# Kernel tuning notes

Hardware: AMD Instinct MI355X
Metric: run time of the kernel (lower is better)

Reference implementation:

```python
import jax, jax.numpy as jnp
import numpy as np

N = 100_000      # nodes
E = 1_600_000    # directed edges (avg degree 16)
F_IN = 128       # num_node_features
H = 8            # heads in conv1
C = 32           # hidden_channels
G = 64           # graphs in batch
NC = 10          # num_classes


def setup_inputs() -> dict:
    key = jax.random.key(0)
    ks = jax.random.split(key, 12)
    gl = lambda k, shape, fan: (jax.random.normal(k, shape, jnp.float32) / np.sqrt(fan)).astype(jnp.float32)
    return {
        "x": jax.random.normal(ks[0], (N, F_IN), jnp.float32),
        "edge_index": jax.random.randint(ks[1], (2, E), 0, N, dtype=jnp.int32),
        "batch": jnp.sort(jax.random.randint(ks[2], (N,), 0, G, dtype=jnp.int32)),
        "W1": gl(ks[3], (F_IN, H * C), F_IN),
        "att_src1": gl(ks[4], (H, C), C),
        "att_dst1": gl(ks[5], (H, C), C),
        "b1": jnp.zeros((H * C,), jnp.float32),
        "W2": gl(ks[6], (H * C, C), H * C),
        "att_src2": gl(ks[7], (1, C), C),
        "att_dst2": gl(ks[8], (1, C), C),
        "b2": jnp.zeros((C,), jnp.float32),
        "Wlin": gl(ks[9], (C, NC), C),
        "blin": jnp.zeros((NC,), jnp.float32),
    }


def gat_conv(x, src, dst, W, att_src, att_dst, bias, heads, ch, concat):
    """PyG GATConv (eval mode): gather, LeakyReLU(0.2) scores, segment softmax over dst, scatter-sum."""
    n = x.shape[0]
    h = (x @ W).reshape(n, heads, ch)                     # [N,H,C]
    a_s = jnp.sum(h * att_src, axis=-1)                   # [N,H]
    a_d = jnp.sum(h * att_dst, axis=-1)                   # [N,H]
    e = jax.nn.leaky_relu(a_s[src] + a_d[dst], 0.2)       # [E,H]
    m = jax.ops.segment_max(e, dst, num_segments=n)       # [N,H], stable softmax
    p = jnp.exp(e - m[dst])
    z = jax.ops.segment_sum(p, dst, num_segments=n)
    coef = p / (z[dst] + 1e-16)                           # [E,H]
    out = jax.ops.segment_sum(coef[:, :, None] * h[src], dst, num_segments=n)  # [N,H,C]
    out = out.reshape(n, heads * ch) if concat else out.mean(axis=1)
    return out + bias


def reference(x, edge_index, batch, W1, att_src1, att_dst1, b1,
              W2, att_src2, att_dst2, b2, Wlin, blin):
    n = x.shape[0]
    loops = jnp.arange(n, dtype=edge_index.dtype)         # GATConv add_self_loops=True
    src = jnp.concatenate([edge_index[0], loops])
    dst = jnp.concatenate([edge_index[1], loops])

    h = gat_conv(x, src, dst, W1, att_src1, att_dst1, b1, H, C, concat=True)
    h = jax.nn.elu(h)                                     # dropout is identity in eval
    h = gat_conv(h, src, dst, W2, att_src2, att_dst2, b2, 1, C, concat=False)

    # global_mean_pool over graph ids
    sums = jax.ops.segment_sum(h, batch, num_segments=G)  # [G,C]
    cnts = jax.ops.segment_sum(jnp.ones((n,), h.dtype), batch, num_segments=G)
    pooled = sums / jnp.maximum(cnts, 1.0)[:, None]

    return pooled @ Wlin + blin                           # [G,NC]
```

## Files before the change

### kernel.cpp

```cpp
#include <hip/hip_runtime.h>
#include <cstdint>

#define NN 100000
#define EE 1600000
#define GG 64
#define FIN 128
#define HC 256
#define NC 10

typedef short v8s __attribute__((ext_vector_type(8)));
typedef float v4f __attribute__((ext_vector_type(4)));

static __device__ __forceinline__ float lrelu(float x) { return x > 0.f ? x : 0.2f * x; }
static __device__ __forceinline__ float bf2f(unsigned short b) {
  return __uint_as_float(((unsigned int)b) << 16);
}
static __device__ __forceinline__ unsigned short f2bf(float f) {
  unsigned int u = __float_as_uint(f);
  unsigned int r = (u + 0x7FFFu + ((u >> 16) & 1u)) >> 16;
  return (unsigned short)r;
}
static __device__ __forceinline__ void unpack2(unsigned int u, float& f0, float& f1) {
  f0 = __uint_as_float(u << 16);
  f1 = __uint_as_float(u & 0xFFFF0000u);
}

__global__ __launch_bounds__(256) void k_prepall(const float* __restrict__ x,
                                                 unsigned short* __restrict__ xb,
                                                 const int* __restrict__ ei,
                                                 int* __restrict__ counts,
                                                 const float* __restrict__ W1,
                                                 unsigned short* __restrict__ W1tg,
                                                 const float* __restrict__ W2,
                                                 unsigned short* __restrict__ W2thi,
                                                 unsigned short* __restrict__ W2tlo) {
  const int b = blockIdx.x;
  const int t = threadIdx.x;
  if (b < 12500) {
    const int idx = b * 256 + t;
    const int i4 = idx * 4;
    float4 v = *(const float4*)(x + i4);
    ushort4 u;
    u.x = f2bf(v.x); u.y = f2bf(v.y); u.z = f2bf(v.z); u.w = f2bf(v.w);
    *(ushort4*)(xb + i4) = u;
    if (idx < EE) atomicAdd(&counts[ei[EE + idx]], 1);
  } else if (b < 12756) {
    const int n = b - 12500;
    if (t < 128) W1tg[n * 128 + t] = f2bf(W1[t * HC + n]);
  } else {
    const int oc = b - 12756;
    float wv = W2[t * 32 + oc];
    unsigned short hi = f2bf(wv);
    W2thi[oc * 256 + t] = hi;
    W2tlo[oc * 256 + t] = f2bf(wv - bf2f(hi));
  }
}

__global__ __launch_bounds__(256) void k_gemm1(const unsigned short* __restrict__ xb,
                                               const unsigned short* __restrict__ W1tg,
                                               const float* __restrict__ att_src1,
                                               const float* __restrict__ att_dst1,
                                               unsigned short* __restrict__ h1b,
                                               float* __restrict__ as1,
                                               float* __restrict__ ad1) {
  const int t = threadIdx.x;
  const int m0 = blockIdx.x * 64;
  const int n0 = blockIdx.y * 128;
  const int hb = blockIdx.y * 4;
  const int lane = t & 63;
  const int wm = t >> 6;
  const int ml = lane & 15;
  const int quad = lane >> 4;
  int row = m0 + wm * 16 + ml; if (row >= NN) row = NN - 1;
  v4f acc[8];
#pragma unroll
  for (int tt = 0; tt < 8; ++tt) acc[tt] = (v4f){0.f, 0.f, 0.f, 0.f};
#pragma unroll
  for (int kk = 0; kk < 4; ++kk) {
    const int k0 = kk * 32 + quad * 8;
    v8s a = *(const v8s*)(xb + (size_t)row * FIN + k0);
#pragma unroll
    for (int tt = 0; tt < 8; ++tt) {
      v8s b = *(const v8s*)(W1tg + (size_t)(n0 + tt * 16 + ml) * FIN + k0);
      acc[tt] = __builtin_amdgcn_mfma_f32_16x16x32_bf16(a, b, acc[tt], 0, 0, 0);
    }
  }
#pragma unroll
  for (int tt = 0; tt < 8; ++tt) {
#pragma unroll
    for (int r = 0; r < 4; ++r) {
      int rg = m0 + wm * 16 + quad * 4 + r;
      if (rg < NN) h1b[(size_t)rg * HC + n0 + tt * 16 + ml] = f2bf(acc[tt][r]);
    }
  }
  float ps[4][4], pd[4][4];
#pragma unroll
  for (int i = 0; i < 4; ++i)
#pragma unroll
    for (int r = 0; r < 4; ++r) { ps[i][r] = 0.f; pd[i][r] = 0.f; }
#pragma unroll
  for (int i = 0; i < 4; ++i) {
#pragma unroll
    for (int half = 0; half < 2; ++half) {
      const int tt = 2 * i + half;
      const float a_s = att_src1[(hb + i) * 32 + half * 16 + ml];
      const float a_d = att_dst1[(hb + i) * 32 + half * 16 + ml];
#pragma unroll
      for (int r = 0; r < 4; ++r) {
        ps[i][r] += acc[tt][r] * a_s;
        pd[i][r] += acc[tt][r] * a_d;
      }
    }
  }
#pragma unroll
  for (int i = 0; i < 4; ++i) {
#pragma unroll
    for (int r = 0; r < 4; ++r) {
      float s = ps[i][r], d = pd[i][r];
      s += __shfl_xor(s, 1, 64); s += __shfl_xor(s, 2, 64);
      s += __shfl_xor(s, 4, 64); s += __shfl_xor(s, 8, 64);
      d += __shfl_xor(d, 1, 64); d += __shfl_xor(d, 2, 64);
      d += __shfl_xor(d, 4, 64); d += __shfl_xor(d, 8, 64);
      ps[i][r] = s; pd[i][r] = d;
    }
  }
  if (ml == 0) {
#pragma unroll
    for (int r = 0; r < 4; ++r) {
      int rg = m0 + wm * 16 + quad * 4 + r;
      if (rg < NN) {
#pragma unroll
        for (int i = 0; i < 4; ++i) {
          as1[rg * 8 + hb + i] = ps[i][r];
          ad1[rg * 8 + hb + i] = pd[i][r];
        }
      }
    }
  }
}

__global__ void k_scan1(const int* __restrict__ counts, int* __restrict__ offs,
                        int* __restrict__ bsums) {
  __shared__ int s[256];
  const int t = threadIdx.x;
  const int i = blockIdx.x * 256 + t;
  int v = (i < NN) ? counts[i] : 0;
  s[t] = v;
  __syncthreads();
  for (int off = 1; off < 256; off <<= 1) {
    int tv = (t >= off) ? s[t - off] : 0;
    __syncthreads();
    s[t] += tv;
    __syncthreads();
  }
  if (i < NN) offs[i] = s[t] - v;
  if (t == 255) bsums[blockIdx.x] = s[255];
}

__global__ void k_scan2(int* __restrict__ bsums, int nb) {
  __shared__ int s[512];
  const int t = threadIdx.x;
  int v = (t < nb) ? bsums[t] : 0;
  s[t] = v;
  __syncthreads();
  for (int off = 1; off < 512; off <<= 1) {
    int tv = (t >= off) ? s[t - off] : 0;
    __syncthreads();
    s[t] += tv;
    __syncthreads();
  }
  if (t < nb) bsums[t] = s[t] - v;
}

__global__ void k_scan3(int* __restrict__ offs, const int* __restrict__ bsums,
                        int* __restrict__ cursor, int* __restrict__ esrc) {
  const int i = blockIdx.x * 256 + threadIdx.x;
  if (i < NN) {
    int v = offs[i] + bsums[i >> 8];
    offs[i] = v;
    cursor[i] = v;
  }
  if (i == 0) offs[NN] = EE;
  if (blockIdx.x == 0 && threadIdx.x < 16) esrc[EE + threadIdx.x] = 0;
}

__global__ void k_scatter(const int* __restrict__ ei, int* __restrict__ cursor,
                          int* __restrict__ esrc) {
  int e = blockIdx.x * 256 + threadIdx.x;
  if (e < EE) {
    int s = ei[e];
    int d = ei[EE + e];
    int p = atomicAdd(&cursor[d], 1);
    esrc[p] = s;
  }
}

__global__ __launch_bounds__(256) void k_agg1(const unsigned short* __restrict__ h1b,
                                              const float* __restrict__ as1,
                                              const float* __restrict__ ad1,
                                              const int* __restrict__ offs,
                                              const int* __restrict__ esrc,
                                              const float* __restrict__ b1,
                                              const unsigned short* __restrict__ W2thi,
                                              const unsigned short* __restrict__ W2tlo,
                                              const float* __restrict__ att_src2,
                                              const float* __restrict__ att_dst2,
                                              unsigned short* __restrict__ h2b,
                                              float* __restrict__ as2,
                                              float* __restrict__ ad2) {
  __shared__ float wl[4][8][36];
  __shared__ __attribute__((aligned(16))) unsigned short o1hi[4][272];
  __shared__ __attribute__((aligned(16))) unsigned short o1lo[4][272];
  const int t = threadIdx.x;
  const int lane = t & 63;
  const int w = t >> 6;
  const int n0 = blockIdx.x * 4;
  const int nu = __builtin_amdgcn_readfirstlane(n0 + w);
  const int hl = lane & 31;
  const int half = lane >> 5;
  const int head = lane >> 3;
  const uint2* __restrict__ h1u2 = (const uint2*)h1b;
  const int start = offs[nu], end = offs[nu + 1];
  const float4 dnA = *(const float4*)(ad1 + (size_t)nu * 8);
  const float4 dnB = *(const float4*)(ad1 + (size_t)nu * 8 + 4);
  const float4 dn4 = (lane & 32) ? dnB : dnA;

  float z, a0, a1, a2, a3;
  {
    float w0 = __expf(lrelu(as1[nu * 8 + head] + ad1[nu * 8 + head]));
    uint2 q = h1u2[(size_t)nu * 64 + lane];
    float f0, f1, f2, f3; unpack2(q.x, f0, f1); unpack2(q.y, f2, f3);
    z = w0; a0 = w0 * f0; a1 = w0 * f1; a2 = w0 * f2; a3 = w0 * f3;
  }
  for (int base = start; base < end; base += 32) {
    const int cnt = min(32, end - base);
    int s = 0;
    if (hl < cnt) s = esrc[base + hl];
    const int hb4 = half << 2;
    const float4 av = *(const float4*)(as1 + (size_t)s * 8 + hb4);
    float w0 = __expf(lrelu(av.x + dn4.x));
    float w1 = __expf(lrelu(av.y + dn4.y));
    float w2 = __expf(lrelu(av.z + dn4.z));
    float w3 = __expf(lrelu(av.w + dn4.w));
    const bool act = hl < cnt;
    wl[w][hb4 + 0][hl] = act ? w0 : 0.f;
    wl[w][hb4 + 1][hl] = act ? w1 : 0.f;
    wl[w][hb4 + 2][hl] = act ? w2 : 0.f;
    wl[w][hb4 + 3][hl] = act ? w3 : 0.f;
    const int cnt4 = (cnt + 3) & ~3;
    int jb = 0;
    for (; jb + 8 <= cnt4; jb += 8) {
      uint2 q[8];
#pragma unroll
      for (int u = 0; u < 8; ++u) {
        const int sj = esrc[base + jb + u];
        q[u] = h1u2[(size_t)sj * 64 + lane];
      }
      const float4 wq0 = *(const float4*)&wl[w][head][jb];
      const float4 wq1 = *(const float4*)&wl[w][head][jb + 4];
      z += ((wq0.x + wq0.y) + (wq0.z + wq0.w)) + ((wq1.x + wq1.y) + (wq1.z + wq1.w));
      float f0, f1, f2, f3;
      unpack2(q[0].x, f0, f1); unpack2(q[0].y, f2, f3);
      a0 += wq0.x * f0; a1 += wq0.x * f1; a2 += wq0.x * f2; a3 += wq0.x * f3;
      unpack2(q[1].x, f0, f1); unpack2(q[1].y, f2, f3);
      a0 += wq0.y * f0; a1 += wq0.y * f1; a2 += wq0.y * f2; a3 += wq0.y * f3;
      unpack2(q[2].x, f0, f1); unpack2(q[2].y, f2, f3);
      a0 += wq0.z * f0; a1 += wq0.z * f1; a2 += wq0.z * f2; a3 += wq0.z * f3;
      unpack2(q[3].x, f0, f1); unpack2(q[3].y, f2, f3);
      a0 += wq0.w * f0; a1 += wq0.w * f1; a2 += wq0.w * f2; a3 += wq0.w * f3;
      unpack2(q[4].x, f0, f1); unpack2(q[4].y, f2, f3);
      a0 += wq1.x * f0; a1 += wq1.x * f1; a2 += wq1.x * f2; a3 += wq1.x * f3;
      unpack2(q[5].x, f0, f1); unpack2(q[5].y, f2, f3);
      a0 += wq1.y * f0; a1 += wq1.y * f1; a2 += wq1.y * f2; a3 += wq1.y * f3;
      unpack2(q[6].x, f0, f1); unpack2(q[6].y, f2, f3);
      a0 += wq1.z * f0; a1 += wq1.z * f1; a2 += wq1.z * f2; a3 += wq1.z * f3;
      unpack2(q[7].x, f0, f1); unpack2(q[7].y, f2, f3);
      a0 += wq1.w * f0; a1 += wq1.w * f1; a2 += wq1.w * f2; a3 += wq1.w * f3;
    }
    if (jb < cnt4) {
      uint2 q[4];
#pragma unroll
      for (int u = 0; u < 4; ++u) {
        const int sj = esrc[base + jb + u];
        q[u] = h1u2[(size_t)sj * 64 + lane];
      }
      const float4 wq0 = *(const float4*)&wl[w][head][jb];
      z += (wq0.x + wq0.y) + (wq0.z + wq0.w);
      float f0, f1, f2, f3;
      unpack2(q[0].x, f0, f1); unpack2(q[0].y, f2, f3);
      a0 += wq0.x * f0; a1 += wq0.x * f1; a2 += wq0.x * f2; a3 += wq0.x * f3;
      unpack2(q[1].x, f0, f1); unpack2(q[1].y, f2, f3);
      a0 += wq0.y * f0; a1 += wq0.y * f1; a2 += wq0.y * f2; a3 += wq0.y * f3;
      unpack2(q[2].x, f0, f1); unpack2(q[2].y, f2, f3);
      a0 += wq0.z * f0; a1 += wq0.z * f1; a2 += wq0.z * f2; a3 += wq0.z * f3;
      unpack2(q[3].x, f0, f1); unpack2(q[3].y, f2, f3);
      a0 += wq0.w * f0; a1 += wq0.w * f1; a2 += wq0.w * f2; a3 += wq0.w * f3;
    }
  }
  {
    const float zi = 1.0f / (z + 1e-16f);
    const float4 bb = *(const float4*)(b1 + 4 * lane);
    float v0 = a0 * zi + bb.x;
    float v1 = a1 * zi + bb.y;
    float v2 = a2 * zi + bb.z;
    float v3 = a3 * zi + bb.w;
    v0 = v0 > 0.f ? v0 : (__expf(v0) - 1.0f);
    v1 = v1 > 0.f ? v1 : (__expf(v1) - 1.0f);
    v2 = v2 > 0.f ? v2 : (__expf(v2) - 1.0f);
    v3 = v3 > 0.f ? v3 : (__expf(v3) - 1.0f);
    ushort4 hh, ll;
    hh.x = f2bf(v0); hh.y = f2bf(v1); hh.z = f2bf(v2); hh.w = f2bf(v3);
    ll.x = f2bf(v0 - bf2f(hh.x));
    ll.y = f2bf(v1 - bf2f(hh.y));
    ll.z = f2bf(v2 - bf2f(hh.z));
    ll.w = f2bf(v3 - bf2f(hh.w));
    *(ushort4*)&o1hi[w][4 * lane] = hh;
    *(ushort4*)&o1lo[w][4 * lane] = ll;
  }
  __syncthreads();
  if (w == 0) {
    const int ml = lane & 15;
    const int quad = lane >> 4;
    const int mr = ml & 3;
    v4f acc[2];
    acc[0] = (v4f){0.f, 0.f, 0.f, 0.f};
    acc[1] = (v4f){0.f, 0.f, 0.f, 0.f};
#pragma unroll
    for (int kk = 0; kk < 8; ++kk) {
      const int k0 = kk * 32 + quad * 8;
      v8s ah = *(const v8s*)&o1hi[mr][k0];
      v8s al = *(const v8s*)&o1lo[mr][k0];
#pragma unroll
      for (int tt = 0; tt < 2; ++tt) {
        v8s bh = *(const v8s*)(W2thi + (size_t)(tt * 16 + ml) * 256 + k0);
        v8s bl = *(const v8s*)(W2tlo + (size_t)(tt * 16 + ml) * 256 + k0);
        acc[tt] = __builtin_amdgcn_mfma_f32_16x16x32_bf16(ah, bh, acc[tt], 0, 0, 0);
        acc[tt] = __builtin_amdgcn_mfma_f32_16x16x32_bf16(al, bh, acc[tt], 0, 0, 0);
        acc[tt] = __builtin_amdgcn_mfma_f32_16x16x32_bf16(ah, bl, acc[tt], 0, 0, 0);
      }
    }
    if (quad == 0) {
      const float s0 = att_src2[ml], s1 = att_src2[16 + ml];
      const float d0 = att_dst2[ml], d1 = att_dst2[16 + ml];
#pragma unroll
      for (int r = 0; r < 4; ++r) {
        const int nn = n0 + r;
        const float h0 = acc[0][r], h1v = acc[1][r];
        h2b[(size_t)nn * 32 + ml] = f2bf(h0);
        h2b[(size_t)nn * 32 + 16 + ml] = f2bf(h1v);
        float ps = h0 * s0 + h1v * s1;
        float pd = h0 * d0 + h1v * d1;
        ps += __shfl_xor(ps, 1, 64); ps += __shfl_xor(ps, 2, 64);
        ps += __shfl_xor(ps, 4, 64); ps += __shfl_xor(ps, 8, 64);
        pd += __shfl_xor(pd, 1, 64); pd += __shfl_xor(pd, 2, 64);
        pd += __shfl_xor(pd, 4, 64); pd += __shfl_xor(pd, 8, 64);
        if (ml == 0) { as2[nn] = ps; ad2[nn] = pd; }
      }
    }
  }
}

__global__ __launch_bounds__(256) void k_agg2(const unsigned short* __restrict__ h2b,
                                              const float* __restrict__ as2,
                                              const float* __restrict__ ad2,
                                              const int* __restrict__ offs,
                                              const int* __restrict__ esrc,
                                              const float* __restrict__ b2,
                                              float* __restrict__ h3) {
  __shared__ int2 swl[4][64];
  const int t = threadIdx.x;
  const int lane = t & 63;
  const int wv = t >> 6;
  const int n = __builtin_amdgcn_readfirstlane(blockIdx.x * 4 + wv);
  const int col = lane & 15;
  const int slot = lane >> 4;
  const unsigned int* __restrict__ h2u = (const unsigned int*)h2b;
  const int start = offs[n], end = offs[n + 1];
  const float adn = ad2[n];
  float z = 0.f, acc0 = 0.f, acc1 = 0.f;
  if (slot == 0) {
    float w0 = __expf(lrelu(as2[n] + adn));
    unsigned int q = h2u[(unsigned)(n * 16 + col)];
    float f0, f1; unpack2(q, f0, f1);
    z = w0; acc0 = w0 * f0; acc1 = w0 * f1;
  }
  for (int base = start; base < end; base += 64) {
    const int cnt = min(64, end - base);
    int s = 0; float wgt = 0.f;
    if (lane < cnt) {
      s = esrc[base + lane];
      wgt = __expf(lrelu(as2[s] + adn));
    }
    swl[wv][lane] = make_int2(s, __float_as_int(wgt));
    const int nit = (cnt + 7) >> 3;
#pragma unroll 2
    for (int j = 0; j < nit; ++j) {
      const int2 p0 = swl[wv][8 * j + slot];
      const int2 p1 = swl[wv][8 * j + 4 + slot];
      const unsigned int q0 = h2u[(unsigned)(p0.x * 16 + col)];
      const unsigned int q1 = h2u[(unsigned)(p1.x * 16 + col)];
      const float wj0 = __int_as_float(p0.y);
      const float wj1 = __int_as_float(p1.y);
      float f0, f1, g0, g1;
      unpack2(q0, f0, f1); unpack2(q1, g0, g1);
      z += wj0 + wj1;
      acc0 += wj0 * f0; acc0 += wj1 * g0;
      acc1 += wj0 * f1; acc1 += wj1 * g1;
    }
  }
  acc0 += __shfl_xor(acc0, 16, 64); acc0 += __shfl_xor(acc0, 32, 64);
  acc1 += __shfl_xor(acc1, 16, 64); acc1 += __shfl_xor(acc1, 32, 64);
  z    += __shfl_xor(z, 16, 64);    z    += __shfl_xor(z, 32, 64);
  if (slot == 0) {
    const float zi = 1.0f / (z + 1e-16f);
    float2 bb = *(const float2*)(b2 + 2 * col);
    float2 o;
    o.x = acc0 * zi + bb.x;
    o.y = acc1 * zi + bb.y;
    *(float2*)(h3 + (size_t)n * 32 + 2 * col) = o;
  }
}

__global__ __launch_bounds__(256) void k_poolfin(const float* __restrict__ h3,
                                                 const int* __restrict__ batch,
                                                 const float* __restrict__ Wlin,
                                                 const float* __restrict__ blin,
                                                 float* __restrict__ out) {
  __shared__ int bounds[2];
  __shared__ float red[8][33];
  __shared__ float mean[32];
  const int g = blockIdx.x;
  const int t = threadIdx.x;
  if (t < 2) {
    int target = g + t;
    int lo = 0, hi = NN;
    while (lo < hi) { int mid = (lo + hi) >> 1; if (batch[mid] < target) lo = mid + 1; else hi = mid; }
    bounds[t] = lo;
  }
  __syncthreads();
  const int lo = bounds[0], hi = bounds[1];
  const int rr = t >> 5, c = t & 31;
  float a = 0.f;
  for (int r = lo + rr; r < hi; r += 8) a += h3[(size_t)r * 32 + c];
  red[rr][c] = a;
  __syncthreads();
  if (rr == 0) {
    float s = 0.f;
#pragma unroll
    for (int i = 0; i < 8; ++i) s += red[i][c];
    float ct = (float)(hi - lo);
    ct = ct > 1.f ? ct : 1.f;
    mean[c] = s / ct;
  }
  __syncthreads();
  if (t < NC) {
    float acc = 0.f;
#pragma unroll
    for (int cc = 0; cc < 32; ++cc) acc += mean[cc] * Wlin[cc * NC + t];
    out[g * NC + t] = acc + blin[t];
  }
}

extern "C" void kernel_launch(void* const* d_in, const int* in_sizes, int n_in,
                              void* d_out, int out_size, void* d_ws, size_t ws_size,
                              hipStream_t stream) {
  const float* x        = (const float*)d_in[0];
  const int*   ei       = (const int*)d_in[1];
  const int*   batch    = (const int*)d_in[2];
  const float* W1       = (const float*)d_in[3];
  const float* att_src1 = (const float*)d_in[4];
  const float* att_dst1 = (const float*)d_in[5];
  const float* b1       = (const float*)d_in[6];
  const float* W2       = (const float*)d_in[7];
  const float* att_src2 = (const float*)d_in[8];
  const float* att_dst2 = (const float*)d_in[9];
  const float* b2       = (const float*)d_in[10];
  const float* Wlin     = (const float*)d_in[11];
  const float* blin     = (const float*)d_in[12];
  float* out = (float*)d_out;
  char* ws = (char*)d_ws;

  unsigned short* h1b   = (unsigned short*)(ws + 0);
  unsigned short* xb    = (unsigned short*)(ws + 51200000);
  float* h3     = (float*)(ws + 51200000);
  float* as1    = (float*)(ws + 76800000);
  float* ad1    = (float*)(ws + 80000000);
  int* counts   = (int*)(ws + 83200000);
  int* offs     = (int*)(ws + 83600000);
  int* cursor   = (int*)(ws + 84000256);
  int* esrc     = (int*)(ws + 84400256);
  int* bsums    = (int*)(ws + 90800320);
  unsigned short* h2b   = (unsigned short*)(ws + 90801920);
  float* as2    = (float*)(ws + 97201920);
  float* ad2    = (float*)(ws + 97601920);
  unsigned short* W1tg  = (unsigned short*)(ws + 98001920);
  unsigned short* W2thi = (unsigned short*)(ws + 98067456);
  unsigned short* W2tlo = (unsigned short*)(ws + 98083840);

  const int nb_scan = (NN + 255) / 256;

  hipMemsetAsync(counts, 0, NN * sizeof(int), stream);
  k_prepall<<<12788, 256, 0, stream>>>(x, xb, ei, counts, W1, W1tg, W2, W2thi, W2tlo);

  dim3 g1((NN + 63) / 64, 2);
  k_gemm1<<<g1, 256, 0, stream>>>(xb, W1tg, att_src1, att_dst1, h1b, as1, ad1);

  k_scan1<<<nb_scan, 256, 0, stream>>>(counts, offs, bsums);
  k_scan2<<<1, 512, 0, stream>>>(bsums, nb_scan);
  k_scan3<<<nb_scan, 256, 0, stream>>>(offs, bsums, cursor, esrc);
  k_scatter<<<(EE + 255) / 256, 256, 0, stream>>>(ei, cursor, esrc);

  k_agg1<<<NN / 4, 256, 0, stream>>>(h1b, as1, ad1, offs, esrc, b1, W2thi, W2tlo,
                                     att_src2, att_dst2, h2b, as2, ad2);

  k_agg2<<<NN / 4, 256, 0, stream>>>(h2b, as2, ad2, offs, esrc, b2, h3);
  k_poolfin<<<GG, 256, 0, stream>>>(h3, batch, Wlin, blin, out);
}
```

Before: 618.6 us.

## Fuse x bf16 conversion into GEMM1, merge scans, widen agg1 blocks

Removes the separate x-to-bf16 pass by converting fp32 x inside k_gemm1 as it loads. That cuts a 51 MB write and read-back, at the cost of reading twice as many bytes per A fragment. Replaces the three-kernel scan with one single-block 1024-thread scan that has each thread serially sum a ~98-element chunk, which saves launches but adds serial, uncoalesced work. Doubles k_agg1 to 8 nodes per 512-thread block so the W2 MFMA projection fills 8 rows instead of 4, amortizing it over more nodes.

```diff
diff --git a/kernel.cpp b/kernel.cpp
--- a/kernel.cpp
+++ b/kernel.cpp
@@ -25,30 +25,23 @@
   f1 = __uint_as_float(u & 0xFFFF0000u);
 }
 
-__global__ __launch_bounds__(256) void k_prepall(const float* __restrict__ x,
-                                                 unsigned short* __restrict__ xb,
-                                                 const int* __restrict__ ei,
-                                                 int* __restrict__ counts,
-                                                 const float* __restrict__ W1,
-                                                 unsigned short* __restrict__ W1tg,
-                                                 const float* __restrict__ W2,
-                                                 unsigned short* __restrict__ W2thi,
-                                                 unsigned short* __restrict__ W2tlo) {
+__global__ __launch_bounds__(256) void k_prep(const int* __restrict__ ei,
+                                              int* __restrict__ counts,
+                                              const float* __restrict__ W1,
+                                              unsigned short* __restrict__ W1tg,
+                                              const float* __restrict__ W2,
+                                              unsigned short* __restrict__ W2thi,
+                                              unsigned short* __restrict__ W2tlo) {
   const int b = blockIdx.x;
   const int t = threadIdx.x;
-  if (b < 12500) {
+  if (b < 6250) {
     const int idx = b * 256 + t;
-    const int i4 = idx * 4;
-    float4 v = *(const float4*)(x + i4);
-    ushort4 u;
-    u.x = f2bf(v.x); u.y = f2bf(v.y); u.z = f2bf(v.z); u.w = f2bf(v.w);
-    *(ushort4*)(xb + i4) = u;
-    if (idx < EE) atomicAdd(&counts[ei[EE + idx]], 1);
-  } else if (b < 12756) {
-    const int n = b - 12500;
+    atomicAdd(&counts[ei[EE + idx]], 1);
+  } else if (b < 6506) {
+    const int n = b - 6250;
     if (t < 128) W1tg[n * 128 + t] = f2bf(W1[t * HC + n]);
   } else {
-    const int oc = b - 12756;
+    const int oc = b - 6506;
     float wv = W2[t * 32 + oc];
     unsigned short hi = f2bf(wv);
     W2thi[oc * 256 + t] = hi;
@@ -56,7 +49,7 @@
   }
 }
 
-__global__ __launch_bounds__(256) void k_gemm1(const unsigned short* __restrict__ xb,
+__global__ __launch_bounds__(256) void k_gemm1(const float* __restrict__ x,
                                                const unsigned short* __restrict__ W1tg,
                                                const float* __restrict__ att_src1,
                                                const float* __restrict__ att_dst1,
@@ -78,7 +71,13 @@
 #pragma unroll
   for (int kk = 0; kk < 4; ++kk) {
     const int k0 = kk * 32 + quad * 8;
-    v8s a = *(const v8s*)(xb + (size_t)row * FIN + k0);
+    const float4 xa = *(const float4*)(x + (size_t)row * FIN + k0);
+    const float4 xc = *(const float4*)(x + (size_t)row * FIN + k0 + 4);
+    v8s a;
+    a[0] = (short)f2bf(xa.x); a[1] = (short)f2bf(xa.y);
+    a[2] = (short)f2bf(xa.z); a[3] = (short)f2bf(xa.w);
+    a[4] = (short)f2bf(xc.x); a[5] = (short)f2bf(xc.y);
+    a[6] = (short)f2bf(xc.z); a[7] = (short)f2bf(xc.w);
 #pragma unroll
     for (int tt = 0; tt < 8; ++tt) {
       v8s b = *(const v8s*)(W1tg + (size_t)(n0 + tt * 16 + ml) * FIN + k0);
@@ -139,49 +138,34 @@
   }
 }
 
-__global__ void k_scan1(const int* __restrict__ counts, int* __restrict__ offs,
-                        int* __restrict__ bsums) {
-  __shared__ int s[256];
-  const int t = threadIdx.x;
-  const int i = blockIdx.x * 256 + t;
-  int v = (i < NN) ? counts[i] : 0;
-  s[t] = v;
+__global__ __launch_bounds__(1024) void k_scanall(const int* __restrict__ counts,
+                                                  int* __restrict__ offs,
+                                                  int* __restrict__ cursor,
+                                                  int* __restrict__ esrc) {
+  __shared__ int ssum[1024];
+  const int t = threadIdx.x;
+  const int CH = (NN + 1023) / 1024;
+  const int lo = t * CH;
+  const int hi = min(lo + CH, NN);
+  int s = 0;
+  for (int i = lo; i < hi; ++i) s += counts[i];
+  ssum[t] = s;
   __syncthreads();
-  for (int off = 1; off < 256; off <<= 1) {
-    int tv = (t >= off) ? s[t - off] : 0;
+  for (int off = 1; off < 1024; off <<= 1) {
+    int v = (t >= off) ? ssum[t - off] : 0;
     __syncthreads();
-    s[t] += tv;
+    ssum[t] += v;
     __syncthreads();
   }
-  if (i < NN) offs[i] = s[t] - v;
-  if (t == 255) bsums[blockIdx.x] = s[255];
-}
-
-__global__ void k_scan2(int* __restrict__ bsums, int nb) {
-  __shared__ int s[512];
-  const int t = threadIdx.x;
-  int v = (t < nb) ? bsums[t] : 0;
-  s[t] = v;
-  __syncthreads();
-  for (int off = 1; off < 512; off <<= 1) {
-    int tv = (t >= off) ? s[t - off] : 0;
-    __syncthreads();
-    s[t] += tv;
-    __syncthreads();
-  }
-  if (t < nb) bsums[t] = s[t] - v;
-}
-
-__global__ void k_scan3(int* __restrict__ offs, const int* __restrict__ bsums,
-                        int* __restrict__ cursor, int* __restrict__ esrc) {
-  const int i = blockIdx.x * 256 + threadIdx.x;
-  if (i < NN) {
-    int v = offs[i] + bsums[i >> 8];
-    offs[i] = v;
-    cursor[i] = v;
-  }
-  if (i == 0) offs[NN] = EE;
-  if (blockIdx.x == 0 && threadIdx.x < 16) esrc[EE + threadIdx.x] = 0;
+  int run = (t == 0) ? 0 : ssum[t - 1];
+  for (int i = lo; i < hi; ++i) {
+    int c = counts[i];
+    offs[i] = run;
+    cursor[i] = run;
+    run += c;
+  }
+  if (t == 0) offs[NN] = EE;
+  if (t < 16) esrc[EE + t] = 0;
 }
 
 __global__ void k_scatter(const int* __restrict__ ei, int* __restrict__ cursor,
@@ -195,7 +179,7 @@
   }
 }
 
-__global__ __launch_bounds__(256) void k_agg1(const unsigned short* __restrict__ h1b,
+__global__ __launch_bounds__(512) void k_agg1(const unsigned short* __restrict__ h1b,
                                               const float* __restrict__ as1,
                                               const float* __restrict__ ad1,
                                               const int* __restrict__ offs,
@@ -208,13 +192,13 @@
                                               unsigned short* __restrict__ h2b,
                                               float* __restrict__ as2,
                                               float* __restrict__ ad2) {
-  __shared__ float wl[4][8][36];
-  __shared__ __attribute__((aligned(16))) unsigned short o1hi[4][272];
-  __shared__ __attribute__((aligned(16))) unsigned short o1lo[4][272];
+  __shared__ float wl[8][8][36];
+  __shared__ __attribute__((aligned(16))) unsigned short o1hi[8][272];
+  __shared__ __attribute__((aligned(16))) unsigned short o1lo[8][272];
   const int t = threadIdx.x;
   const int lane = t & 63;
   const int w = t >> 6;
-  const int n0 = blockIdx.x * 4;
+  const int n0 = blockIdx.x * 8;
   const int nu = __builtin_amdgcn_readfirstlane(n0 + w);
   const int hl = lane & 31;
   const int half = lane >> 5;
@@ -321,7 +305,7 @@
   if (w == 0) {
     const int ml = lane & 15;
     const int quad = lane >> 4;
-    const int mr = ml & 3;
+    const int mr = ml & 7;
     v4f acc[2];
     acc[0] = (v4f){0.f, 0.f, 0.f, 0.f};
     acc[1] = (v4f){0.f, 0.f, 0.f, 0.f};
@@ -339,12 +323,12 @@
         acc[tt] = __builtin_amdgcn_mfma_f32_16x16x32_bf16(ah, bl, acc[tt], 0, 0, 0);
       }
     }
-    if (quad == 0) {
+    if (quad < 2) {
       const float s0 = att_src2[ml], s1 = att_src2[16 + ml];
       const float d0 = att_dst2[ml], d1 = att_dst2[16 + ml];
 #pragma unroll
       for (int r = 0; r < 4; ++r) {
-        const int nn = n0 + r;
+        const int nn = n0 + quad * 4 + r;
         const float h0 = acc[0][r], h1v = acc[1][r];
         h2b[(size_t)nn * 32 + ml] = f2bf(h0);
         h2b[(size_t)nn * 32 + 16 + ml] = f2bf(h1v);
@@ -481,36 +465,30 @@
   char* ws = (char*)d_ws;
 
   unsigned short* h1b   = (unsigned short*)(ws + 0);
-  unsigned short* xb    = (unsigned short*)(ws + 51200000);
-  float* h3     = (float*)(ws + 51200000);
-  float* as1    = (float*)(ws + 76800000);
-  float* ad1    = (float*)(ws + 80000000);
-  int* counts   = (int*)(ws + 83200000);
-  int* offs     = (int*)(ws + 83600000);
-  int* cursor   = (int*)(ws + 84000256);
-  int* esrc     = (int*)(ws + 84400256);
-  int* bsums    = (int*)(ws + 90800320);
-  unsigned short* h2b   = (unsigned short*)(ws + 90801920);
-  float* as2    = (float*)(ws + 97201920);
-  float* ad2    = (float*)(ws + 97601920);
-  unsigned short* W1tg  = (unsigned short*)(ws + 98001920);
-  unsigned short* W2thi = (unsigned short*)(ws + 98067456);
-  unsigned short* W2tlo = (unsigned short*)(ws + 98083840);
-
-  const int nb_scan = (NN + 255) / 256;
+  float* as1    = (float*)(ws + 51200000);
+  float* ad1    = (float*)(ws + 54400000);
+  int* counts   = (int*)(ws + 57600000);
+  int* offs     = (int*)(ws + 58000000);
+  int* cursor   = (int*)(ws + 58400256);
+  int* esrc     = (int*)(ws + 58800256);
+  unsigned short* h2b   = (unsigned short*)(ws + 65200384);
+  float* as2    = (float*)(ws + 71600384);
+  float* ad2    = (float*)(ws + 72000384);
+  unsigned short* W1tg  = (unsigned short*)(ws + 72400384);
+  unsigned short* W2thi = (unsigned short*)(ws + 72465920);
+  unsigned short* W2tlo = (unsigned short*)(ws + 72482304);
+  float* h3     = (float*)(ws + 72498688);
 
   hipMemsetAsync(counts, 0, NN * sizeof(int), stream);
-  k_prepall<<<12788, 256, 0, stream>>>(x, xb, ei, counts, W1, W1tg, W2, W2thi, W2tlo);
+  k_prep<<<6538, 256, 0, stream>>>(ei, counts, W1, W1tg, W2, W2thi, W2tlo);
 
   dim3 g1((NN + 63) / 64, 2);
-  k_gemm1<<<g1, 256, 0, stream>>>(xb, W1tg, att_src1, att_dst1, h1b, as1, ad1);
-
-  k_scan1<<<nb_scan, 256, 0, stream>>>(counts, offs, bsums);
-  k_scan2<<<1, 512, 0, stream>>>(bsums, nb_scan);
-  k_scan3<<<nb_scan, 256, 0, stream>>>(offs, bsums, cursor, esrc);
+  k_gemm1<<<g1, 256, 0, stream>>>(x, W1tg, att_src1, att_dst1, h1b, as1, ad1);
+
+  k_scanall<<<1, 1024, 0, stream>>>(counts, offs, cursor, esrc);
   k_scatter<<<(EE + 255) / 256, 256, 0, stream>>>(ei, cursor, esrc);
 
-  k_agg1<<<NN / 4, 256, 0, stream>>>(h1b, as1, ad1, offs, esrc, b1, W2thi, W2tlo,
+  k_agg1<<<NN / 8, 512, 0, stream>>>(h1b, as1, ad1, offs, esrc, b1, W2thi, W2tlo,
                                      att_src2, att_dst2, h2b, as2, ad2);
 
   k_agg2<<<NN / 4, 256, 0, stream>>>(h2b, as2, ad2, offs, esrc, b2, h3);
```

Result: slower. 816.1 us (+31.9%).
